# Kernel optimization log

Measured on AMD Instinct MI355X. Metric: run time of the kernel, lower is better.

## Reference

```python
import jax, jax.numpy as jnp
import numpy as np

N_QUBITS = 8
N_PAIRS = 4
PAIRS = [(2 * p, 2 * p + 1) for p in range(N_PAIRS)]
STRENGTH = 0.8
DIM = 2 ** N_QUBITS


def _apply_1q_full(st, G, q):
    # st: (2,)*n complex64 state, G: [2,2] gate on qubit q (qubit 0 = most significant)
    out = jnp.tensordot(G, st, axes=([1], [q]))
    return jnp.moveaxis(out, 0, q)


def _apply_ctrl_full(st, G, c, t):
    # controlled-G: apply G on target axis t only where control axis c == 1
    s0 = jnp.take(st, 0, axis=c)
    s1 = jnp.take(st, 1, axis=c)
    t2 = t if t < c else t - 1
    s1 = jnp.moveaxis(jnp.tensordot(G, s1, axes=([1], [t2])), 0, t2)
    return jnp.stack([s0, s1], axis=c)


def _entangled_base():
    # |0...0> -> H on q1, partial CNOT (controlled-RX(pi*strength)) on (q1,q2) per pair
    st = jnp.zeros((2,) * N_QUBITS, jnp.complex64).at[(0,) * N_QUBITS].set(1.0)
    H = jnp.array([[1.0, 1.0], [1.0, -1.0]], jnp.complex64) / np.float32(np.sqrt(2.0))
    th = np.float32(np.pi * STRENGTH)
    c, s = np.float32(np.cos(th / 2)), np.float32(np.sin(th / 2))
    RX = jnp.array([[c, -1j * s], [-1j * s, c]], jnp.complex64)
    for q1, q2 in PAIRS:
        st = _apply_1q_full(st, H, q1)
        st = _apply_ctrl_full(st, RX, q1, q2)
    return st.reshape(-1)


def _rx(theta):
    # RX(theta) = [[cos t/2, -i sin t/2], [-i sin t/2, cos t/2]], batched over theta shape
    cz = jnp.cos(0.5 * theta).astype(jnp.complex64)
    sz = (-1j) * jnp.sin(0.5 * theta).astype(jnp.complex64)
    return jnp.stack([jnp.stack([cz, sz], -1), jnpp_stack_fix(sz, cz)], -2) if False else jnp.stack([jnp.stack([cz, sz], -1), jnp.stack([sz, cz], -1)], -2)


def _rz(theta):
    ph = (0.5j) * theta.astype(jnp.complex64)
    e0, e1 = jnp.exp(-ph), jnp.exp(ph)
    z = jnp.zeros_like(e0)
    return jnp.stack([jnp.stack([e0, z], -1), jnp.stack([z, e1], -1)], -2)


def _quantum_scores(k_states):
    # k_states: [B,S,2*n_qubits] -> expected pair-agreement score [B,S]
    B, S, _ = k_states.shape
    k = k_states.reshape(B, S, N_QUBITS, 2)
    eye = jnp.eye(2, dtype=jnp.complex64)
    st = jnp.broadcast_to(_entangled_base(), (B, S, DIM))  # fresh entangled register per (b,j)
    for q in range(N_QUBITS):
        th_x, th_z = k[:, :, q, 0], k[:, :, q, 1]
        Gx = jnp.where((th_x > 0)[..., None, None], _rx(th_x), eye)
        Gz = jnp.where((th_z > 0)[..., None, None], _rz(th_z), eye)
        G = jnp.einsum('bsij,bsjk->bsik', Gz, Gx)  # RX applied first, then RZ
        L = 2 ** q
        R = DIM // (2 * L)
        stv = st.reshape(B, S, L, 2, R)
        st = jnp.einsum('bsij,bsljr->bslir', G, stv).reshape(B, S, DIM)
    probs = (st.real ** 2 + st.imag ** 2).reshape((B, S) + (2,) * N_QUBITS)
    score = jnp.zeros((B, S), probs.dtype)
    for q1, q2 in PAIRS:
        axes = tuple(2 + a for a in range(N_QUBITS) if a not in (q1, q2))
        marg = probs.sum(axis=axes)  # [B,S,2,2] joint marginal of the pair
        score = score + marg[..., 0, 0] + marg[..., 1, 1]  # P(measure equal)
    return score / N_PAIRS


def reference(query, key, value, Wq, bq, Wk, bk, Wv, bv, Wo, bo):
    q_states = query @ Wq + bq  # computed as in original forward (unused by scores)
    k_states = key @ Wk + bk    # [B,S,2*n_qubits]
    v_states = value @ Wv + bv  # [B,S,d_model]
    B, S, _ = k_states.shape
    score = _quantum_scores(k_states)  # [B,S]; deterministic expected agreement
    # original loop makes score[b,i,j] independent of i under independent per-(b,i,j) sims
    attn = jnp.broadcast_to(score[:, None, :], (B, S, S))
    w = jax.nn.softmax(attn, axis=-1)
    out = jnp.einsum('bij,bjd->bid', w, v_states)
    return out @ Wo + bo


def setup_inputs() -> dict:
    rng = jax.random.key(0)
    ks = jax.random.split(rng, 8)
    B, S, D = 8, 2048, 512
    nq2 = 2 * N_QUBITS
    f = jax.random.normal
    return {
        'query': f(ks[0], (B, S, D), jnp.float32),
        'key': f(ks[1], (B, S, D), jnp.float32),
        'value': f(ks[2], (B, S, D), jnp.float32),
        'Wq': f(ks[3], (D, nq2), jnp.float32) * 0.05,
        'bq': jnp.zeros((nq2,), jnp.float32),
        'Wk': f(ks[4], (D, nq2), jnp.float32) * 0.05,
        'bk': jnp.zeros((nq2,), jnp.float32),
        'Wv': f(ks[5], (D, D), jnp.float32) * 0.05,
        'bv': jnp.zeros((D,), jnp.float32),
        'Wo': f(ks[6], (D, D), jnp.float32) * 0.05,
        'bo': jnp.zeros((D,), jnp.float32),
    }
```

## Files before the change

kernel.cpp:

```cpp
#include <hip/hip_runtime.h>
#include <math.h>

#define DEV __device__ __forceinline__

struct C2 { float x, y; };
DEV C2 cmul(C2 a, C2 b){ return {a.x*b.x - a.y*b.y, a.x*b.y + a.y*b.x}; }
DEV C2 cadd(C2 a, C2 b){ return {a.x+b.x, a.y+b.y}; }
DEV C2 cscale(C2 a, float s){ return {a.x*s, a.y*s}; }
DEV C2 cnegi(C2 a){ return {a.y, -a.x}; }

__global__ __launch_bounds__(512, 4) void k_score_wsum(const float* __restrict__ key,
                                                       const float* __restrict__ Wk,
                                                       const float* __restrict__ bk,
                                                       const float* __restrict__ value,
                                                       float* __restrict__ partial,
                                                       float* __restrict__ partialw)
{
    const int c = blockIdx.x;
    const int b = blockIdx.y;
    const int t = threadIdx.x;
    const int lane = t & 63;
    const int wv   = t >> 6;
    const int h    = wv & 1;
    const int pr   = wv >> 1;
    const int base = b * 2048 + c * 32;
    const int wrow0 = pr * 8;

    __shared__ float  kslds[2][32][16];
    __shared__ float4 red[8][128];
    __shared__ float  wsums[4];

    float4 wk[4][4];
    #pragma unroll
    for (int jj = 0; jj < 4; ++jj) {
        const float4* w0 = (const float4*)(Wk + (h * 256 + 4 * lane + jj) * 16);
        #pragma unroll
        for (int q = 0; q < 4; ++q) wk[jj][q] = w0[q];
    }
    const float c0 = 0.30901699437494745f;
    const float s0 = 0.9510565162951535f;

    const float4* kp = (const float4*)(key + (size_t)(base + wrow0) * 512);
    float4 cur = kp[h * 64 + lane];
    #pragma unroll
    for (int j = 0; j < 8; ++j) {
        float4 nx;
        if (j < 7) nx = kp[(j + 1) * 128 + h * 64 + lane];
        float el[4] = {cur.x, cur.y, cur.z, cur.w};
        float acc[16];
        #pragma unroll
        for (int k = 0; k < 16; ++k) acc[k] = 0.f;
        #pragma unroll
        for (int jj = 0; jj < 4; ++jj) {
            #pragma unroll
            for (int q = 0; q < 4; ++q) {
                acc[4*q+0] = fmaf(el[jj], wk[jj][q].x, acc[4*q+0]);
                acc[4*q+1] = fmaf(el[jj], wk[jj][q].y, acc[4*q+1]);
                acc[4*q+2] = fmaf(el[jj], wk[jj][q].z, acc[4*q+2]);
                acc[4*q+3] = fmaf(el[jj], wk[jj][q].w, acc[4*q+3]);
            }
        }
        #pragma unroll
        for (int s = 0; s < 4; ++s) {
            const int m = 1 << s;
            const int bbit = (lane >> s) & 1;
            #pragma unroll
            for (int jj = 0; jj < (16 >> (s + 1)); ++jj) {
                float send = bbit ? acc[2*jj] : acc[2*jj+1];
                float keep = bbit ? acc[2*jj+1] : acc[2*jj];
                acc[jj] = keep + __shfl_xor(send, m);
            }
        }
        float ks = acc[0];
        ks += __shfl_xor(ks, 16);
        ks += __shfl_xor(ks, 32);
        if (lane < 16) kslds[h][wrow0 + j][lane] = ks;
        cur = nx;
    }

    const int vrow0 = wrow0 + h * 4;
    const float4* vp = (const float4*)(value + (size_t)(base + vrow0) * 512);
    float4 vreg[8];
    #pragma unroll
    for (int j = 0; j < 4; ++j) {
        vreg[2*j]   = vp[j * 128 + lane];
        vreg[2*j+1] = vp[j * 128 + 64 + lane];
    }
    __syncthreads();

    const int p  = (lane >> 3) & 3;
    const int jr = lane & 7;
    float4 k0 = *(const float4*)&kslds[0][wrow0 + jr][4 * p];
    float4 k1 = *(const float4*)&kslds[1][wrow0 + jr][4 * p];
    float4 bk4 = ((const float4*)bk)[p];
    float ax = k0.x + k1.x + bk4.x, az = k0.y + k1.y + bk4.y;
    float bx = k0.z + k1.z + bk4.z, bz = k0.w + k1.w + bk4.w;
    float cxa = 1.f, sxa = 0.f; if (ax > 0.f){ sxa = __sinf(0.5f*ax); cxa = __cosf(0.5f*ax); }
    float cpa = 1.f, spa = 0.f; if (az > 0.f){ spa = __sinf(0.5f*az); cpa = __cosf(0.5f*az); }
    float cxb = 1.f, sxb = 0.f; if (bx > 0.f){ sxb = __sinf(0.5f*bx); cxb = __cosf(0.5f*bx); }
    float cpb = 1.f, spb = 0.f; if (bz > 0.f){ spb = __sinf(0.5f*bz); cpb = __cosf(0.5f*bz); }
    C2 A00{cpa*cxa, -spa*cxa}, A01{-spa*sxa, -cpa*sxa};
    C2 A10{spa*sxa, -cpa*sxa}, A11{ cpa*cxa,  spa*cxa};
    C2 B00{cpb*cxb, -spb*cxb}, B01{-spb*sxb, -cpb*sxb};
    C2 B10{spb*sxb, -cpb*sxb}, B11{ cpb*cxb,  spb*cxb};
    C2 u = cadd(cmul(B00, cadd(A00, cscale(A01, c0))),
                cscale(cnegi(cmul(A01, B01)), s0));
    C2 v = cadd(cmul(B10, cadd(A10, cscale(A11, c0))),
                cscale(cnegi(cmul(A11, B11)), s0));
    float ps = u.x*u.x + u.y*u.y + v.x*v.x + v.y*v.y;
    ps += __shfl_xor(ps, 8);
    ps += __shfl_xor(ps, 16);
    float w_all = __expf(ps * 0.125f);

    if (h == 0) {
        float sw = w_all;
        sw += __shfl_xor(sw, 1); sw += __shfl_xor(sw, 2); sw += __shfl_xor(sw, 4);
        if (lane == 0) wsums[pr] = sw;
    }

    float4 aA = {0.f,0.f,0.f,0.f}, aB = {0.f,0.f,0.f,0.f};
    #pragma unroll
    for (int j = 0; j < 4; ++j) {
        float wj = __shfl(w_all, h * 4 + j);
        float4 v0 = vreg[2*j], v1 = vreg[2*j+1];
        aA.x = fmaf(wj, v0.x, aA.x); aA.y = fmaf(wj, v0.y, aA.y);
        aA.z = fmaf(wj, v0.z, aA.z); aA.w = fmaf(wj, v0.w, aA.w);
        aB.x = fmaf(wj, v1.x, aB.x); aB.y = fmaf(wj, v1.y, aB.y);
        aB.z = fmaf(wj, v1.z, aB.z); aB.w = fmaf(wj, v1.w, aB.w);
    }
    red[wv][lane] = aA;
    red[wv][64 + lane] = aB;
    __syncthreads();
    if (t < 128) {
        float4 q0 = red[0][t], q1 = red[1][t], q2 = red[2][t], q3 = red[3][t];
        float4 q4 = red[4][t], q5 = red[5][t], q6 = red[6][t], q7 = red[7][t];
        float4 o = { q0.x+q1.x+q2.x+q3.x+q4.x+q5.x+q6.x+q7.x,
                     q0.y+q1.y+q2.y+q3.y+q4.y+q5.y+q6.y+q7.y,
                     q0.z+q1.z+q2.z+q3.z+q4.z+q5.z+q6.z+q7.z,
                     q0.w+q1.w+q2.w+q3.w+q4.w+q5.w+q6.w+q7.w };
        ((float4*)partial)[((size_t)b * 64 + c) * 128 + t] = o;
    }
    if (t == 0)
        partialw[b * 64 + c] = wsums[0] + wsums[1] + wsums[2] + wsums[3];
}

__global__ __launch_bounds__(512) void k_tail(const float* __restrict__ partial,
                                              const float* __restrict__ partialw,
                                              const float* __restrict__ Wv,
                                              const float* __restrict__ bv,
                                              const float* __restrict__ Wo,
                                              const float* __restrict__ bo,
                                              float* __restrict__ out)
{
    const int sl = blockIdx.x;
    const int b  = blockIdx.y;
    const int t  = threadIdx.x;

    __shared__ float cbuf[512];
    __shared__ float xbuf[512];
    __shared__ float frl[512];
    __shared__ float sS;

    if (t < 64) {
        float s = partialw[b * 64 + t];
        s += __shfl_xor(s, 1);  s += __shfl_xor(s, 2);
        s += __shfl_xor(s, 4);  s += __shfl_xor(s, 8);
        s += __shfl_xor(s, 16); s += __shfl_xor(s, 32);
        if (t == 0) sS = 1.f / s;
    }

    {
        float cs = 0.f;
        const float* pp = partial + (size_t)b * 32768 + t;
        #pragma unroll 8
        for (int cc = 0; cc < 64; ++cc) cs += pp[(size_t)cc * 512];
        cbuf[t] = cs;
    }
    __syncthreads();
    const float invS = sS;

    {
        float a0 = 0.f, a1 = 0.f, a2 = 0.f, a3 = 0.f;
        #pragma unroll 4
        for (int e = 0; e < 512; e += 4) {
            a0 = fmaf(cbuf[e],   Wv[(size_t)e * 512 + t],     a0);
            a1 = fmaf(cbuf[e+1], Wv[(size_t)(e+1) * 512 + t], a1);
            a2 = fmaf(cbuf[e+2], Wv[(size_t)(e+2) * 512 + t], a2);
            a3 = fmaf(cbuf[e+3], Wv[(size_t)(e+3) * 512 + t], a3);
        }
        xbuf[t] = ((a0 + a1) + (a2 + a3)) * invS + bv[t];
    }
    __syncthreads();

    {
        float a0 = 0.f, a1 = 0.f, a2 = 0.f, a3 = 0.f;
        #pragma unroll 4
        for (int e = 0; e < 512; e += 4) {
            a0 = fmaf(xbuf[e],   Wo[(size_t)e * 512 + t],     a0);
            a1 = fmaf(xbuf[e+1], Wo[(size_t)(e+1) * 512 + t], a1);
            a2 = fmaf(xbuf[e+2], Wo[(size_t)(e+2) * 512 + t], a2);
            a3 = fmaf(xbuf[e+3], Wo[(size_t)(e+3) * 512 + t], a3);
        }
        frl[t] = ((a0 + a1) + (a2 + a3)) + bo[t];
    }
    __syncthreads();

    {
        const int col4 = t & 127, rg = t >> 7;
        float4 val = ((const float4*)frl)[col4];
        float4* o4 = (float4*)out
                   + ((size_t)b * 2048 + sl * 256 + rg * 64) * 128 + col4;
        #pragma unroll 8
        for (int r = 0; r < 64; ++r) o4[(size_t)r * 128] = val;
    }
}

extern "C" void kernel_launch(void* const* d_in, const int* in_sizes, int n_in,
                              void* d_out, int out_size, void* d_ws, size_t ws_size,
                              hipStream_t stream) {
    const float* key   = (const float*)d_in[1];
    const float* value = (const float*)d_in[2];
    const float* Wk    = (const float*)d_in[5];
    const float* bk    = (const float*)d_in[6];
    const float* Wv    = (const float*)d_in[7];
    const float* bv    = (const float*)d_in[8];
    const float* Wo    = (const float*)d_in[9];
    const float* bo    = (const float*)d_in[10];
    float* out = (float*)d_out;
    float* ws  = (float*)d_ws;

    float* partial  = ws;
    float* partialw = ws + 262144;

    k_score_wsum<<<dim3(64, 8), 512, 0, stream>>>(key, Wk, bk, value,
                                                  partial, partialw);
    k_tail      <<<dim3(8, 8),  512, 0, stream>>>(partial, partialw,
                                                  Wv, bv, Wo, bo, out);
}
```

Before: 189.7 us.

## Split tail into matvec kernel and separate wide broadcast-store kernel

Splits the old tail kernel into two. The new k_mid keeps the 8x8 grid, but each block computes only a 64-column slice of the Wo projection, splitting the reduction across 8 thread groups instead of computing all 512 columns redundantly. A new k_bcast kernel with 512 blocks then writes the broadcast output rows, spreading the large output store over many more CUs. Accumulator unrolling is also widened in the partial-sum and Wv loops. The cost is one extra kernel launch and a small workspace round trip.

```diff
diff --git a/kernel.cpp b/kernel.cpp
--- a/kernel.cpp
+++ b/kernel.cpp
@@ -144,21 +144,21 @@
         partialw[b * 64 + c] = wsums[0] + wsums[1] + wsums[2] + wsums[3];
 }
 
-__global__ __launch_bounds__(512) void k_tail(const float* __restrict__ partial,
-                                              const float* __restrict__ partialw,
-                                              const float* __restrict__ Wv,
-                                              const float* __restrict__ bv,
-                                              const float* __restrict__ Wo,
-                                              const float* __restrict__ bo,
-                                              float* __restrict__ out)
+__global__ __launch_bounds__(512) void k_mid(const float* __restrict__ partial,
+                                             const float* __restrict__ partialw,
+                                             const float* __restrict__ Wv,
+                                             const float* __restrict__ bv,
+                                             const float* __restrict__ Wo,
+                                             const float* __restrict__ bo,
+                                             float* __restrict__ frow)
 {
-    const int sl = blockIdx.x;
+    const int dt = blockIdx.x;
     const int b  = blockIdx.y;
     const int t  = threadIdx.x;
 
     __shared__ float cbuf[512];
     __shared__ float xbuf[512];
-    __shared__ float frl[512];
+    __shared__ float red[512];
     __shared__ float sS;
 
     if (t < 64) {
@@ -170,49 +170,70 @@
     }
 
     {
-        float cs = 0.f;
+        float c0 = 0.f, c1 = 0.f, c2 = 0.f, c3 = 0.f;
         const float* pp = partial + (size_t)b * 32768 + t;
+        #pragma unroll
+        for (int cc = 0; cc < 64; cc += 4) {
+            c0 += pp[(size_t)cc * 512];
+            c1 += pp[(size_t)(cc + 1) * 512];
+            c2 += pp[(size_t)(cc + 2) * 512];
+            c3 += pp[(size_t)(cc + 3) * 512];
+        }
+        cbuf[t] = (c0 + c1) + (c2 + c3);
+    }
+    __syncthreads();
+    const float invS = sS;
+
+    {
+        float a0=0.f,a1=0.f,a2=0.f,a3=0.f,a4=0.f,a5=0.f,a6=0.f,a7=0.f;
         #pragma unroll 8
-        for (int cc = 0; cc < 64; ++cc) cs += pp[(size_t)cc * 512];
-        cbuf[t] = cs;
-    }
-    __syncthreads();
-    const float invS = sS;
-
-    {
-        float a0 = 0.f, a1 = 0.f, a2 = 0.f, a3 = 0.f;
-        #pragma unroll 4
-        for (int e = 0; e < 512; e += 4) {
+        for (int e = 0; e < 512; e += 8) {
             a0 = fmaf(cbuf[e],   Wv[(size_t)e * 512 + t],     a0);
             a1 = fmaf(cbuf[e+1], Wv[(size_t)(e+1) * 512 + t], a1);
             a2 = fmaf(cbuf[e+2], Wv[(size_t)(e+2) * 512 + t], a2);
             a3 = fmaf(cbuf[e+3], Wv[(size_t)(e+3) * 512 + t], a3);
-        }
-        xbuf[t] = ((a0 + a1) + (a2 + a3)) * invS + bv[t];
+            a4 = fmaf(cbuf[e+4], Wv[(size_t)(e+4) * 512 + t], a4);
+            a5 = fmaf(cbuf[e+5], Wv[(size_t)(e+5) * 512 + t], a5);
+            a6 = fmaf(cbuf[e+6], Wv[(size_t)(e+6) * 512 + t], a6);
+            a7 = fmaf(cbuf[e+7], Wv[(size_t)(e+7) * 512 + t], a7);
+        }
+        xbuf[t] = (((a0+a1)+(a2+a3)) + ((a4+a5)+(a6+a7))) * invS + bv[t];
     }
     __syncthreads();
 
     {
-        float a0 = 0.f, a1 = 0.f, a2 = 0.f, a3 = 0.f;
-        #pragma unroll 4
-        for (int e = 0; e < 512; e += 4) {
-            a0 = fmaf(xbuf[e],   Wo[(size_t)e * 512 + t],     a0);
-            a1 = fmaf(xbuf[e+1], Wo[(size_t)(e+1) * 512 + t], a1);
-            a2 = fmaf(xbuf[e+2], Wo[(size_t)(e+2) * 512 + t], a2);
-            a3 = fmaf(xbuf[e+3], Wo[(size_t)(e+3) * 512 + t], a3);
-        }
-        frl[t] = ((a0 + a1) + (a2 + a3)) + bo[t];
-    }
-    __syncthreads();
-
-    {
-        const int col4 = t & 127, rg = t >> 7;
-        float4 val = ((const float4*)frl)[col4];
-        float4* o4 = (float4*)out
-                   + ((size_t)b * 2048 + sl * 256 + rg * 64) * 128 + col4;
+        const int dl = t & 63, g = t >> 6;
+        const int d  = dt * 64 + dl;
+        const float* Wc = Wo + (size_t)(g * 64) * 512 + d;
+        const float* xg = xbuf + g * 64;
+        float a0=0.f,a1=0.f,a2=0.f,a3=0.f;
         #pragma unroll 8
-        for (int r = 0; r < 64; ++r) o4[(size_t)r * 128] = val;
-    }
+        for (int e = 0; e < 64; e += 4) {
+            a0 = fmaf(xg[e],   Wc[(size_t)e * 512],       a0);
+            a1 = fmaf(xg[e+1], Wc[(size_t)(e+1) * 512],   a1);
+            a2 = fmaf(xg[e+2], Wc[(size_t)(e+2) * 512],   a2);
+            a3 = fmaf(xg[e+3], Wc[(size_t)(e+3) * 512],   a3);
+        }
+        red[t] = (a0 + a1) + (a2 + a3);
+    }
+    __syncthreads();
+    if (t < 64) {
+        float r = red[t]       + red[t + 64]  + red[t + 128] + red[t + 192]
+                + red[t + 256] + red[t + 320] + red[t + 384] + red[t + 448];
+        frow[b * 512 + dt * 64 + t] = r + bo[dt * 64 + t];
+    }
+}
+
+__global__ __launch_bounds__(256) void k_bcast(const float* __restrict__ frow,
+                                               float* __restrict__ out)
+{
+    int s = blockIdx.x, b = blockIdx.y, t = threadIdx.x;
+    const int col4 = t & 127, h = t >> 7;
+    float4 val = ((const float4*)frow)[b * 128 + col4];
+    float4* o4 = (float4*)out
+               + ((size_t)b * 2048 + s * 32 + h * 16) * 128 + col4;
+    #pragma unroll
+    for (int r = 0; r < 16; ++r) o4[(size_t)r * 128] = val;
 }
 
 extern "C" void kernel_launch(void* const* d_in, const int* in_sizes, int n_in,
@@ -231,9 +252,11 @@
 
     float* partial  = ws;
     float* partialw = ws + 262144;
+    float* frow     = ws + 262656;
 
     k_score_wsum<<<dim3(64, 8), 512, 0, stream>>>(key, Wk, bk, value,
                                                   partial, partialw);
-    k_tail      <<<dim3(8, 8),  512, 0, stream>>>(partial, partialw,
-                                                  Wv, bv, Wo, bo, out);
-}
+    k_mid       <<<dim3(8, 8),  512, 0, stream>>>(partial, partialw,
+                                                  Wv, bv, Wo, bo, frow);
+    k_bcast     <<<dim3(64, 8), 256, 0, stream>>>(frow, out);
+}
```

Measured after the change: 168.8 us. 1.12x faster.
